# Kernel tuning notes

Measured on AMD Instinct MI355X. Metric: run time of the kernel, lower is better.

## Reference

```python
import jax, jax.numpy as jnp
import numpy as np
import math

B, H, T, N = 2, 4, 2048, 2048
THETA = 2.0 ** 16


def get_freqs(n: int, theta: float) -> jnp.ndarray:
    # quantize arange to multiples of 2, matching torch (t/2).floor()*2
    t = jnp.arange(n, dtype=jnp.float32)
    q = jnp.floor(t / 2.0) * 2.0
    return 1.0 / theta ** (q / n) / (2.0 * math.pi)


def rope(phases: jnp.ndarray, v: jnp.ndarray) -> jnp.ndarray:
    # v: [B,H,T,N]; phases: [T,N] (broadcast). Interleaved pair rotation.
    ph = (phases % 1.0) * (2.0 * math.pi)
    c, s = jnp.cos(ph), jnp.sin(ph)
    v2 = v.reshape(*v.shape[:-1], -1, 2)           # [...,N/2,2]
    v_rot = jnp.stack((-v2[..., 1], v2[..., 0]), axis=-1).reshape(v.shape)
    return (v * c + v_rot * s).astype(v.dtype)


def setup_inputs() -> dict:
    key = jax.random.key(0)
    kq, kv = jax.random.split(key)
    Q = jax.random.normal(kq, (B, H, T, N), dtype=jnp.float32)
    V = jax.random.normal(kv, (B, H, T, N), dtype=jnp.float32)
    return {"Q": Q, "V": V}


def reference(Q, V):
    Tlen = Q.shape[2]
    n = Q.shape[3]
    freqs = get_freqs(n, THETA)                               # [N]
    phases = jnp.arange(Tlen, dtype=jnp.float32)[:, None] * freqs[None, :]  # [T,N]
    QR = rope(phases, Q)                                      # K is Q -> KR = QR
    scores = jnp.einsum('bhtn,bhsn->bhts', QR, QR)            # [B,H,T,T]
    # strictly-causal mask: keep s < t (tril with diagonal=-1)
    mask = jnp.tril(jnp.ones((Tlen, Tlen), dtype=bool), k=-1)
    scores = jnp.where(mask, scores, 0.0)
    out = jnp.einsum('bhts,bhsn->bhtn', scores, V)
    return out
```

## Files before the change

kernel.cpp:

```cpp
#include <hip/hip_runtime.h>
#include <hip/hip_bf16.h>

#define TDIM 2048
#define NDIM 2048
#define BHN  8
#define LD   2048

typedef __attribute__((ext_vector_type(8))) short bf16x8;
typedef __attribute__((ext_vector_type(4))) float f32x4;
typedef unsigned short us;

static __device__ __forceinline__ us f2bf(float x) {
  union { __hip_bfloat16 h; us u; } cv;
  cv.h = __float2bfloat16(x);
  return cv.u;
}

__global__ __launch_bounds__(256) void rope_kernel(const float* __restrict__ Q,
                                                   us* __restrict__ QR,
                                                   int total8) {
  int idx = blockIdx.x * blockDim.x + threadIdx.x;
  if (idx >= total8) return;
  long base = (long)idx * 8;
  int n = (int)(base & (NDIM - 1));
  int t = (int)((base >> 11) & (TDIM - 1));
  const float4* p = reinterpret_cast<const float4*>(Q + base);
  float4 v0 = p[0], v1 = p[1];
  float q[8] = {v0.x, v0.y, v0.z, v0.w, v1.x, v1.y, v1.z, v1.w};
  us r[8];
  float tf = (float)t;
#pragma unroll
  for (int pr = 0; pr < 4; ++pr) {
    int nn = n + pr * 2;
    float freq = __builtin_exp2f((float)nn * (-1.0f / 128.0f)) * 0.15915494309189535f;
    float ph = tf * freq;
    ph = ph - __builtin_floorf(ph);
    float c = __builtin_amdgcn_cosf(ph);
    float s = __builtin_amdgcn_sinf(ph);
    float e = q[2 * pr], o = q[2 * pr + 1];
    r[2 * pr]     = f2bf(e * c - o * s);
    r[2 * pr + 1] = f2bf(o * c + e * s);
  }
  union { us usv[8]; bf16x8 v; } pk;
#pragma unroll
  for (int i = 0; i < 8; ++i) pk.usv[i] = r[i];
  *reinterpret_cast<bf16x8*>(QR + base) = pk.v;
}

__global__ __launch_bounds__(256) void vtrans_kernel(const float* __restrict__ V,
                                                     us* __restrict__ VT,
                                                     us* __restrict__ Sflag) {
  __shared__ float tile[32][33];
  if (Sflag != nullptr && blockIdx.x == 0 && blockIdx.y == 0 && blockIdx.z == 0 &&
      threadIdx.x == 0 && threadIdx.y == 0) {
    for (int h = 0; h < BHN; ++h) {
      unsigned* f = (unsigned*)(Sflag + (long)h * TDIM * LD + 1792);
      for (int i = 0; i < 36; ++i)
        __hip_atomic_store(&f[i], 0u, __ATOMIC_RELAXED, __HIP_MEMORY_SCOPE_AGENT);
    }
  }
  int bh = blockIdx.z;
  int n0 = blockIdx.x * 32, t0 = blockIdx.y * 32;
  const float* Vp = V + (long)bh * TDIM * NDIM;
  us* Tp = VT + (long)bh * TDIM * NDIM;
  int tx = threadIdx.x, ty = threadIdx.y;
#pragma unroll
  for (int i = 0; i < 4; ++i)
    tile[ty + i * 8][tx] = Vp[(long)(t0 + ty + i * 8) * NDIM + n0 + tx];
  __syncthreads();
#pragma unroll
  for (int i = 0; i < 4; ++i)
    Tp[(long)(n0 + ty + i * 8) * TDIM + t0 + tx] = f2bf(tile[tx][ty + i * 8]);
}

template <int PASS>
__device__ __forceinline__ void run_tile(const us* __restrict__ A,
                                         const us* __restrict__ B,
                                         void* __restrict__ Cbase,
                                         us* __restrict__ lds,
                                         int rt, int ct, int tid,
                                         unsigned* __restrict__ fh) {
  const int lane = tid & 63, wid = tid >> 6;
  const int wr = wid >> 2, wc = wid & 3;
  const int l15 = lane & 15, l4 = lane >> 4;
  const int row0 = rt * 256, col0 = ct * 256;
  const int kts = (PASS == 0) ? 32 : (rt + 1) * 4;
  const int fbase = rt * (rt + 1) / 2;

  auto waitflag = [&](int idx) {
    if (tid == 0) {
      while (__hip_atomic_fetch_add(&fh[idx], 0u, __ATOMIC_RELAXED,
                                    __HIP_MEMORY_SCOPE_AGENT) == 0u)
        __builtin_amdgcn_s_sleep(4);
    }
    __builtin_amdgcn_s_barrier();
  };

  f32x4 acc[8][4];
#pragma unroll
  for (int m = 0; m < 8; ++m)
#pragma unroll
    for (int n = 0; n < 4; ++n) acc[m][n] = (f32x4){0.f, 0.f, 0.f, 0.f};

  auto stage = [&](int half , int t) {
    const us* g0 = (half < 2) ? A : B;
    const int tr0 = (half < 2) ? row0 : col0;
    const int h = half & 1;
    us* lb = lds + ((half < 2) ? 0 : 32768) + (t & 1) * 16384;
    const int k0 = t * 64;
#pragma unroll
    for (int r = 0; r < 2; ++r) {
      int off = r * 512 + tid;
      int row = off >> 3;
      int ch = off & 7;
      int chl = ch ^ (row & 7);
      const us* g = g0 + (long)(tr0 + h * 128 + row) * LD + (k0 + chl * 8);
      us* l = lb + h * 8192 + off * 8;
      __builtin_amdgcn_global_load_lds(
          (const __attribute__((address_space(1))) unsigned int*)g,
          (__attribute__((address_space(3))) unsigned int*)l, 16, 0, 0);
    }
  };
  auto ldA = [&](int b, int m, int ks) -> bf16x8 {
    int row = wr * 128 + m * 16 + l15;
    int ch = (ks * 4 + l4) ^ (row & 7);
    return *reinterpret_cast<const bf16x8*>(lds + b * 16384 + row * 64 + ch * 8);
  };
  auto ldB = [&](int b, int n, int ks) -> bf16x8 {
    int row = wc * 64 + n * 16 + l15;
    int ch = (ks * 4 + l4) ^ (row & 7);
    return *reinterpret_cast<const bf16x8*>(lds + 32768 + b * 16384 + row * 64 + ch * 8);
  };

  if constexpr (PASS == 1) waitflag(fbase);

  stage(0, 0); stage(1, 0); stage(2, 0); stage(3, 0);
  if (1 < kts) { stage(2, 1); stage(3, 1); }
  asm volatile("s_waitcnt vmcnt(4)" ::: "memory");
  __builtin_amdgcn_s_barrier();
  __builtin_amdgcn_sched_barrier(0);

  bf16x8 af[4][2], bfr[4][2];
  for (int t = 0; t < kts; ++t) {
    const int b = t & 1;
    if constexpr (PASS == 1) {
      int tn = t + 1;
      if (tn < kts && (tn & 3) == 0) waitflag(fbase + (tn >> 2));
    }
#pragma unroll
    for (int m = 0; m < 4; ++m) { af[m][0] = ldA(b, m, 0); af[m][1] = ldA(b, m, 1); }
#pragma unroll
    for (int n = 0; n < 2; ++n) { bfr[n][0] = ldB(b, n, 0); bfr[n][1] = ldB(b, n, 1); }
    if (t + 1 < kts) stage(0, t + 1);
    __builtin_amdgcn_s_barrier();
    asm volatile("s_waitcnt lgkmcnt(0)" ::: "memory");
    __builtin_amdgcn_sched_barrier(0);
    __builtin_amdgcn_s_setprio(1);
#pragma unroll
    for (int m = 0; m < 4; ++m)
#pragma unroll
      for (int n = 0; n < 2; ++n)
#pragma unroll
        for (int ks = 0; ks < 2; ++ks)
          acc[m][n] = __builtin_amdgcn_mfma_f32_16x16x32_bf16(af[m][ks], bfr[n][ks], acc[m][n], 0, 0, 0);
    __builtin_amdgcn_s_setprio(0);
    __builtin_amdgcn_sched_barrier(0);
    __builtin_amdgcn_s_barrier();
#pragma unroll
    for (int n = 2; n < 4; ++n) { bfr[n][0] = ldB(b, n, 0); bfr[n][1] = ldB(b, n, 1); }
    if (t + 1 < kts) stage(1, t + 1);
    __builtin_amdgcn_s_barrier();
    asm volatile("s_waitcnt lgkmcnt(0)" ::: "memory");
    __builtin_amdgcn_sched_barrier(0);
    __builtin_amdgcn_s_setprio(1);
#pragma unroll
    for (int m = 0; m < 4; ++m)
#pragma unroll
      for (int n = 2; n < 4; ++n)
#pragma unroll
        for (int ks = 0; ks < 2; ++ks)
          acc[m][n] = __builtin_amdgcn_mfma_f32_16x16x32_bf16(af[m][ks], bfr[n][ks], acc[m][n], 0, 0, 0);
    __builtin_amdgcn_s_setprio(0);
    __builtin_amdgcn_sched_barrier(0);
    __builtin_amdgcn_s_barrier();
#pragma unroll
    for (int m = 0; m < 4; ++m) { af[m][0] = ldA(b, m + 4, 0); af[m][1] = ldA(b, m + 4, 1); }
    if (t + 2 < kts) stage(2, t + 2);
    __builtin_amdgcn_s_barrier();
    asm volatile("s_waitcnt lgkmcnt(0)" ::: "memory");
    __builtin_amdgcn_sched_barrier(0);
    __builtin_amdgcn_s_setprio(1);
#pragma unroll
    for (int m = 0; m < 4; ++m)
#pragma unroll
      for (int n = 0; n < 2; ++n)
#pragma unroll
        for (int ks = 0; ks < 2; ++ks)
          acc[m + 4][n] = __builtin_amdgcn_mfma_f32_16x16x32_bf16(af[m][ks], bfr[n][ks], acc[m + 4][n], 0, 0, 0);
    __builtin_amdgcn_s_setprio(0);
    __builtin_amdgcn_sched_barrier(0);
    __builtin_amdgcn_s_barrier();
    if (t + 2 < kts) stage(3, t + 2);
    __builtin_amdgcn_s_setprio(1);
#pragma unroll
    for (int m = 0; m < 4; ++m)
#pragma unroll
      for (int n = 2; n < 4; ++n)
#pragma unroll
        for (int ks = 0; ks < 2; ++ks)
          acc[m + 4][n] = __builtin_amdgcn_mfma_f32_16x16x32_bf16(af[m][ks], bfr[n][ks], acc[m + 4][n], 0, 0, 0);
    __builtin_amdgcn_s_setprio(0);
    if (t + 2 < kts) { asm volatile("s_waitcnt vmcnt(4)" ::: "memory"); }
    else             { asm volatile("s_waitcnt vmcnt(0)" ::: "memory"); }
    __builtin_amdgcn_sched_barrier(0);
    __builtin_amdgcn_s_barrier();
    __builtin_amdgcn_sched_barrier(0);
  }

  if constexpr (PASS == 0) {
    us* C = (us*)Cbase;
    const bool diag = (rt == ct);
#pragma unroll
    for (int m = 0; m < 8; ++m) {
      int r0 = row0 + wr * 128 + m * 16 + l4 * 4;
#pragma unroll
      for (int n = 0; n < 4; ++n) {
        int cc = col0 + wc * 64 + n * 16 + l15;
#pragma unroll
        for (int j = 0; j < 4; ++j) {
          int tt = r0 + j;
          float v = acc[m][n][j];
          if (diag && cc >= tt) v = 0.0f;
          C[(long)tt * LD + cc] = f2bf(v);
        }
      }
    }
    __syncthreads();
    if (tid == 0)
      __hip_atomic_store(&fh[fbase + ct], 1u, __ATOMIC_RELEASE,
                         __HIP_MEMORY_SCOPE_AGENT);
  } else {
    float* C = (float*)Cbase;
#pragma unroll
    for (int m = 0; m < 8; ++m) {
      int r0 = row0 + wr * 128 + m * 16 + l4 * 4;
#pragma unroll
      for (int n = 0; n < 4; ++n) {
        int cc = col0 + wc * 64 + n * 16 + l15;
#pragma unroll
        for (int j = 0; j < 4; ++j)
          C[(long)(r0 + j) * LD + cc] = acc[m][n][j];
      }
    }
  }
}

__global__ __launch_bounds__(512, 2) void gemm_fused(const us* __restrict__ QR,
                                                     const us* __restrict__ VT,
                                                     us* __restrict__ S,
                                                     float* __restrict__ Out) {
  extern __shared__ us lds[];
  const int b = (int)blockIdx.x;
  const int head = b & 7, u = b >> 3;
  const int tid = (int)threadIdx.x;
  const us* QRh = QR + (long)head * TDIM * LD;
  const us* VTh = VT + (long)head * TDIM * LD;
  us* Sh = S + (long)head * TDIM * LD;
  float* Oh = Out + (long)head * TDIM * LD;
  unsigned* fh = (unsigned*)(Sh + 1792);

  const int nt0 = (u < 4) ? 2 : 1;
#pragma unroll 1
  for (int i = 0; i < nt0; ++i) {
    int tri = (i == 0) ? u : 32 + u;
    int rt = 0;
    while ((rt + 1) * (rt + 2) / 2 <= tri) ++rt;
    int ct = tri - rt * (rt + 1) / 2;
    run_tile<0>(QRh, QRh, Sh, lds, rt, ct, tid, fh);
  }

  int prt[3], pct[3], np;
  if (u < 4)       { prt[0] = 1; pct[0] = u; np = 1; }
  else if (u < 8)  { prt[0] = 1; pct[0] = u; prt[1] = 7; pct[1] = u - 4; np = 2; }
  else if (u < 12) { prt[0] = 0; pct[0] = 2 * (u - 8); prt[1] = 0; pct[1] = 2 * (u - 8) + 1;
                     prt[2] = 7; pct[2] = u - 4; np = 3; }
  else if (u < 20) { prt[0] = 2; pct[0] = u - 12; prt[1] = 6; pct[1] = u - 12; np = 2; }
  else if (u < 28) { prt[0] = 3; pct[0] = u - 20; prt[1] = 5; pct[1] = u - 20; np = 2; }
  else             { prt[0] = 4; pct[0] = 2 * (u - 28); prt[1] = 4; pct[1] = 2 * (u - 28) + 1; np = 2; }
#pragma unroll 1
  for (int i = 0; i < np; ++i)
    run_tile<1>(Sh, VTh, Oh, lds, prt[i], pct[i], tid, fh);
}

template <int PASS>
__global__ __launch_bounds__(512, 2) void gemm256(
    const us* __restrict__ Abase, const us* __restrict__ Bbase,
    void* __restrict__ Cbase, int nh) {
  extern __shared__ us lds[];
  int bid = (int)blockIdx.x;
  int head, rt = 0, ct, cls = 0;
  if constexpr (PASS == 0) {
    head = bid % nh;
    int tri = bid / nh;
    rt = 0;
    while ((rt + 1) * (rt + 2) / 2 <= tri) ++rt;
    ct = tri - rt * (rt + 1) / 2;
  } else {
    head = bid % nh;
    int rem = bid / nh;
    ct = rem & 7;
    cls = rem >> 3;
  }
  const us* A = Abase + (long)head * TDIM * LD;
  const us* B = Bbase + (long)head * TDIM * LD;
  us* Sh = (us*)Cbase + (long)head * TDIM * LD;
  const int tid = (int)threadIdx.x;
  const int NSEG = (PASS == 0) ? 1 : 2;
#pragma unroll 1
  for (int seg = 0; seg < NSEG; ++seg) {
    int rts = rt, cts = ct;
    if constexpr (PASS == 1) { rts = seg ? cls : 7 - cls; cts = ct; }
    if constexpr (PASS == 0) {
      run_tile<0>(A, A, Sh, lds, rts, cts, tid,
                  (unsigned*)(Sh + 1792));
    } else {
      float* Oh = (float*)Cbase + (long)head * TDIM * LD;
      run_tile<1>(A, B, Oh, lds, rts, cts, tid,
                  (unsigned*)((us*)Abase + (long)head * TDIM * LD + 1792));
    }
  }
}

extern "C" void kernel_launch(void* const* d_in, const int* in_sizes, int n_in,
                              void* d_out, int out_size, void* d_ws, size_t ws_size,
                              hipStream_t stream) {
  const float* Q = (const float*)d_in[0];
  const float* V = (const float*)d_in[1];
  float* Out = (float*)d_out;
  char* ws = (char*)d_ws;
  const long TN = (long)TDIM * NDIM;
  const size_t BUF = (size_t)BHN * TN * 2;
  const size_t PERBH = (size_t)TN * 2;
  const int SHMEM = 131072;

  hipFuncSetAttribute(reinterpret_cast<const void*>(&gemm_fused),
                      hipFuncAttributeMaxDynamicSharedMemorySize, SHMEM);
  hipFuncSetAttribute(reinterpret_cast<const void*>(&gemm256<0>),
                      hipFuncAttributeMaxDynamicSharedMemorySize, SHMEM);
  hipFuncSetAttribute(reinterpret_cast<const void*>(&gemm256<1>),
                      hipFuncAttributeMaxDynamicSharedMemorySize, SHMEM);

  if (ws_size >= 3 * BUF) {
    us* QRb = (us*)ws;
    us* VbT = (us*)(ws + BUF);
    us* S   = (us*)(ws + 2 * BUF);
    int total8 = (int)(BHN * TN / 8);
    rope_kernel<<<dim3(total8 / 256), dim3(256), 0, stream>>>(Q, QRb, total8);
    vtrans_kernel<<<dim3(64, 64, 8), dim3(32, 8), 0, stream>>>(V, VbT, S);
    void* args[] = {(void*)&QRb, (void*)&VbT, (void*)&S, (void*)&Out};
    hipError_t ce = hipLaunchCooperativeKernel(
        reinterpret_cast<const void*>(&gemm_fused), dim3(256), dim3(512),
        args, (unsigned)SHMEM, stream);
    if (ce != hipSuccess) {
      (void)hipGetLastError();
      gemm256<0><<<dim3(36 * BHN), dim3(512), SHMEM, stream>>>(QRb, QRb, S, BHN);
      gemm256<1><<<dim3(32 * BHN), dim3(512), SHMEM, stream>>>(S, VbT, Out, BHN);
    }
  } else {
    us* QR0 = (us*)ws;
    us* VT0 = (us*)(ws + PERBH);
    us* S0  = (us*)(ws + 2 * PERBH);
    int total8 = (int)(TN / 8);
    for (int bh = 0; bh < BHN; ++bh) {
      rope_kernel<<<dim3(total8 / 256), dim3(256), 0, stream>>>(Q + bh * TN, QR0, total8);
      vtrans_kernel<<<dim3(64, 64, 1), dim3(32, 8), 0, stream>>>(V + bh * TN, VT0, S0);
      gemm256<0><<<dim3(36), dim3(512), SHMEM, stream>>>(QR0, QR0, S0, 1);
      gemm256<1><<<dim3(32), dim3(512), SHMEM, stream>>>(S0, VT0, Out + bh * TN, 1);
    }
  }
}
```

Baseline: 276.4 us.

## Replace static pass-1 tile assignment with atomic work queue in fused GEMM

The fused kernel now computes the score tiles in reverse row order, largest rows first. Each block then pulls output tiles from a per-head atomic counter instead of following a fixed per-block assignment. The flag-clearing loop is extended to reset the new queue counter. This aims to balance the triangular workload across blocks dynamically and cut tail idle time. In exchange it adds an atomic and two barriers per tile, and blocks may spin longer on dependency flags depending on the order they pick tiles.

```diff
diff --git a/kernel.cpp b/kernel.cpp
--- a/kernel.cpp
+++ b/kernel.cpp
@@ -55,7 +55,7 @@
       threadIdx.x == 0 && threadIdx.y == 0) {
     for (int h = 0; h < BHN; ++h) {
       unsigned* f = (unsigned*)(Sflag + (long)h * TDIM * LD + 1792);
-      for (int i = 0; i < 36; ++i)
+      for (int i = 0; i < 40; ++i)
         __hip_atomic_store(&f[i], 0u, __ATOMIC_RELAXED, __HIP_MEMORY_SCOPE_AGENT);
     }
   }
@@ -268,28 +268,37 @@
   us* Sh = S + (long)head * TDIM * LD;
   float* Oh = Out + (long)head * TDIM * LD;
   unsigned* fh = (unsigned*)(Sh + 1792);
-
-  const int nt0 = (u < 4) ? 2 : 1;
-#pragma unroll 1
-  for (int i = 0; i < nt0; ++i) {
-    int tri = (i == 0) ? u : 32 + u;
-    int rt = 0;
-    while ((rt + 1) * (rt + 2) / 2 <= tri) ++rt;
-    int ct = tri - rt * (rt + 1) / 2;
-    run_tile<0>(QRh, QRh, Sh, lds, rt, ct, tid, fh);
-  }
-
-  int prt[3], pct[3], np;
-  if (u < 4)       { prt[0] = 1; pct[0] = u; np = 1; }
-  else if (u < 8)  { prt[0] = 1; pct[0] = u; prt[1] = 7; pct[1] = u - 4; np = 2; }
-  else if (u < 12) { prt[0] = 0; pct[0] = 2 * (u - 8); prt[1] = 0; pct[1] = 2 * (u - 8) + 1;
-                     prt[2] = 7; pct[2] = u - 4; np = 3; }
-  else if (u < 20) { prt[0] = 2; pct[0] = u - 12; prt[1] = 6; pct[1] = u - 12; np = 2; }
-  else if (u < 28) { prt[0] = 3; pct[0] = u - 20; prt[1] = 5; pct[1] = u - 20; np = 2; }
-  else             { prt[0] = 4; pct[0] = 2 * (u - 28); prt[1] = 4; pct[1] = 2 * (u - 28) + 1; np = 2; }
-#pragma unroll 1
-  for (int i = 0; i < np; ++i)
-    run_tile<1>(Sh, VTh, Oh, lds, prt[i], pct[i], tid, fh);
+  unsigned* qc = fh + 36;
+
+  int rt0, ct0;
+  if (u < 8)       { rt0 = 7; ct0 = u; }
+  else if (u < 15) { rt0 = 6; ct0 = u - 8; }
+  else if (u < 21) { rt0 = 5; ct0 = u - 15; }
+  else if (u < 26) { rt0 = 4; ct0 = u - 21; }
+  else if (u < 30) { rt0 = 3; ct0 = u - 26; }
+  else             { rt0 = 2; ct0 = (u == 30) ? 0 : 2; }
+  run_tile<0>(QRh, QRh, Sh, lds, rt0, ct0, tid, fh);
+  if (u >= 28) {
+    int rt1, ct1;
+    if (u == 28)      { rt1 = 1; ct1 = 0; }
+    else if (u == 29) { rt1 = 1; ct1 = 1; }
+    else if (u == 30) { rt1 = 2; ct1 = 1; }
+    else              { rt1 = 0; ct1 = 0; }
+    run_tile<0>(QRh, QRh, Sh, lds, rt1, ct1, tid, fh);
+  }
+
+  for (;;) {
+    if (tid == 0) {
+      unsigned i = __hip_atomic_fetch_add(qc, 1u, __ATOMIC_RELAXED,
+                                          __HIP_MEMORY_SCOPE_AGENT);
+      *(volatile unsigned*)lds = i;
+    }
+    __syncthreads();
+    unsigned i = *(volatile unsigned*)lds;
+    __syncthreads();
+    if (i >= 64) break;
+    run_tile<1>(Sh, VTh, Oh, lds, 7 - (int)(i >> 3), (int)(i & 7), tid, fh);
+  }
 }
 
 template <int PASS>
@@ -321,8 +330,7 @@
     int rts = rt, cts = ct;
     if constexpr (PASS == 1) { rts = seg ? cls : 7 - cls; cts = ct; }
     if constexpr (PASS == 0) {
-      run_tile<0>(A, A, Sh, lds, rts, cts, tid,
-                  (unsigned*)(Sh + 1792));
+      run_tile<0>(A, A, Sh, lds, rts, cts, tid, (unsigned*)(Sh + 1792));
     } else {
       float* Oh = (float*)Cbase + (long)head * TDIM * LD;
       run_tile<1>(A, B, Oh, lds, rts, cts, tid,
```

Result: faster. 263.9 us (-4.5%).
